# Optimization experiments

Hardware: AMD Instinct MI355X
Metric: run time of the kernel (lower is better)

The kernel has to match this reference:

```python
import jax, jax.numpy as jnp
import numpy as np

N_NODES = 50000
N_EDGES = 800000


def _sage(x, src, dst, Wl, bl, Wr):
    # mean-aggregate neighbor features (messages flow src -> dst), then linear
    msg = x[src]                                              # [E, d_in]
    s = jax.ops.segment_sum(msg, dst, num_segments=N_NODES)   # [N, d_in]
    cnt = jax.ops.segment_sum(jnp.ones((src.shape[0],), x.dtype), dst,
                              num_segments=N_NODES)           # [N]
    agg = s / jnp.maximum(cnt, 1.0)[:, None]
    return agg @ Wl.T + bl + x @ Wr.T


def setup_inputs() -> dict:
    key = jax.random.key(0)
    ks = jax.random.split(key, 10)
    d_in, h = 128, 64
    def w(k, o, i):
        return jax.random.normal(k, (o, i), jnp.float32) * (1.0 / np.sqrt(i))
    return {
        "x": jax.random.normal(ks[0], (N_NODES, d_in), jnp.float32),
        "edge_index": jax.random.randint(ks[1], (2, N_EDGES), 0, N_NODES, jnp.int64),
        "Wl1": w(ks[2], h, d_in), "bl1": jnp.zeros((h,), jnp.float32), "Wr1": w(ks[3], h, d_in),
        "Wl2": w(ks[4], 2 * h, h), "bl2": jnp.zeros((2 * h,), jnp.float32), "Wr2": w(ks[5], 2 * h, h),
        "Wl3": w(ks[6], 2 * h, 2 * h), "bl3": jnp.zeros((2 * h,), jnp.float32), "Wr3": w(ks[7], 2 * h, 2 * h),
        "Wl4": w(ks[8], h, 2 * h), "bl4": jnp.zeros((h,), jnp.float32), "Wr4": w(ks[9], h, 2 * h),
    }


def reference(x, edge_index, Wl1, bl1, Wr1, Wl2, bl2, Wr2, Wl3, bl3, Wr3, Wl4, bl4, Wr4):
    src, dst = edge_index[0], edge_index[1]
    h = jax.nn.relu(_sage(x, src, dst, Wl1, bl1, Wr1))
    h = jax.nn.relu(_sage(h, src, dst, Wl2, bl2, Wr2))
    h = jax.nn.relu(_sage(h, src, dst, Wl3, bl3, Wr3))
    h = _sage(h, src, dst, Wl4, bl4, Wr4)
    return h
```

## Files before the change

kernel.cpp:

```cpp
#include <hip/hip_runtime.h>

#define NN 50000
#define NE 800000
#define GB 391
#define NBUK 196
#define PB 128
#define CH 6250
#define HLEN (NBUK * PB)
#define SAB (HLEN / 256)

typedef __attribute__((ext_vector_type(8))) short short8v;
typedef __attribute__((ext_vector_type(4))) float float4v;

__device__ __forceinline__ int uni(int v) { return __builtin_amdgcn_readfirstlane(v); }
__device__ __forceinline__ unsigned short f2bf(float f) {
    unsigned u = __float_as_uint(f);
    return (unsigned short)((u + 0x7FFFu + ((u >> 16) & 1u)) >> 16);
}
__device__ __forceinline__ float bf2f(unsigned short h) {
    return __uint_as_float(((unsigned)h) << 16);
}

__global__ __launch_bounds__(256) void hist_kernel(const int* __restrict__ dst,
                                                   int* __restrict__ H) {
    __shared__ int h[NBUK];
    const int t = threadIdx.x;
    const int b = blockIdx.x;
    if (t < NBUK) h[t] = 0;
    __syncthreads();
    const int e0 = b * CH;
    for (int i = t; i < CH; i += 256) {
        int e = e0 + i;
        if (e < NE) atomicAdd(&h[dst[e] >> 8], 1);
    }
    __syncthreads();
    if (t < NBUK) H[t * PB + b] = h[t];
}

__global__ __launch_bounds__(256) void scanA_kernel(const int* __restrict__ a,
                                                    int* __restrict__ part) {
    __shared__ int red[256];
    const int t = threadIdx.x;
    red[t] = a[blockIdx.x * 256 + t];
    __syncthreads();
#pragma unroll
    for (int d = 128; d > 0; d >>= 1) {
        if (t < d) red[t] += red[t + d];
        __syncthreads();
    }
    if (t == 0) part[blockIdx.x] = red[0];
}

__global__ __launch_bounds__(128) void scanB_kernel(int* __restrict__ part) {
    __shared__ int ps[128];
    const int t = threadIdx.x;
    ps[t] = (t < SAB) ? part[t] : 0;
    __syncthreads();
#pragma unroll
    for (int d = 1; d < 128; d <<= 1) {
        int v = (t >= d) ? ps[t - d] : 0;
        __syncthreads();
        ps[t] += v;
        __syncthreads();
    }
    if (t < SAB) part[t] = (t == 0) ? 0 : ps[t - 1];
}

__global__ __launch_bounds__(256) void scanC_kernel(int* __restrict__ a,
                                                    const int* __restrict__ part) {
    __shared__ int ps[256];
    const int t = threadIdx.x;
    const int i = blockIdx.x * 256 + t;
    const int c = a[i];
    ps[t] = c;
    __syncthreads();
#pragma unroll
    for (int d = 1; d < 256; d <<= 1) {
        int v = (t >= d) ? ps[t - d] : 0;
        __syncthreads();
        ps[t] += v;
        __syncthreads();
    }
    a[i] = part[blockIdx.x] + ps[t] - c;
}

__global__ __launch_bounds__(256) void partition_kernel(const int* __restrict__ src,
                                                        const int* __restrict__ dst,
                                                        const int* __restrict__ Hs,
                                                        unsigned* __restrict__ tmp) {
    __shared__ int cur[NBUK];
    const int t = threadIdx.x;
    const int b = blockIdx.x;
    if (t < NBUK) cur[t] = Hs[t * PB + b];
    __syncthreads();
    const int e0 = b * CH;
    for (int i = t; i < CH; i += 256) {
        int e = e0 + i;
        if (e < NE) {
            const int d = dst[e];
            const int k = d >> 8;
            const int pos = atomicAdd(&cur[k], 1);
            tmp[pos] = (unsigned)src[e] | ((unsigned)(d & 255) << 16);
        }
    }
}

__global__ __launch_bounds__(256) void finalize_kernel(const unsigned* __restrict__ tmp,
                                                       const int* __restrict__ Hs,
                                                       int* __restrict__ off,
                                                       int* __restrict__ cnt,
                                                       float* __restrict__ inv,
                                                       int* __restrict__ srcs) {
    __shared__ int hist[256];
    __shared__ int ps[256];
    __shared__ int cur[256];
    const int t = threadIdx.x;
    const int k = blockIdx.x;
    const int s0 = Hs[k * PB];
    const int end = (k == NBUK - 1) ? NE : Hs[(k + 1) * PB];
    const int m = end - s0;
    hist[t] = 0;
    __syncthreads();
    for (int i = t; i < m; i += 256) {
        atomicAdd(&hist[(tmp[s0 + i] >> 16) & 255], 1);
    }
    __syncthreads();
    const int c = hist[t];
    ps[t] = c;
    __syncthreads();
#pragma unroll
    for (int d = 1; d < 256; d <<= 1) {
        int v = (t >= d) ? ps[t - d] : 0;
        __syncthreads();
        ps[t] += v;
        __syncthreads();
    }
    const int ex = ps[t] - c;
    const int node = k * 256 + t;
    if (node < NN) {
        off[node] = s0 + ex;
        cnt[node] = c;
        inv[node] = 1.0f / (float)max(c, 1);
    }
    cur[t] = s0 + ex;
    __syncthreads();
    for (int i = t; i < m; i += 256) {
        const unsigned u = tmp[s0 + i];
        const int p = atomicAdd(&cur[(u >> 16) & 255], 1);
        srcs[p] = (int)(u & 0xFFFFu);
    }
}

template<int D, int MODE, int DUALB>
__global__ __launch_bounds__(256) void gather_kernel(
    const unsigned short* __restrict__ yb, int ys, const int* __restrict__ srcs,
    const int* __restrict__ off, const int* __restrict__ cnt,
    const float* __restrict__ inv, const float* __restrict__ pre, int ps,
    float* __restrict__ out, int os, unsigned short* __restrict__ outb) {
    const int w = (blockIdx.x * blockDim.x + threadIdx.x) >> 6;
    const int lane = threadIdx.x & 63;
    if (w >= NN) return;
    const int o = uni(off[w]);
    const int n = uni(cnt[w]);
    const int h = lane >> 5;
    const int l = lane & 31;

    float a0 = 0.0f, a1 = 0.0f, a2 = 0.0f, a3 = 0.0f;
    int i = 0;
    for (; i + 8 <= n; i += 8) {
        int e0 = srcs[o + i + h];
        int e1 = srcs[o + i + 2 + h];
        int e2 = srcs[o + i + 4 + h];
        int e3 = srcs[o + i + 6 + h];
        if constexpr (D == 64) {
            const ushort2 v0 = *reinterpret_cast<const ushort2*>(&yb[(size_t)e0 * ys + 2 * l]);
            const ushort2 v1 = *reinterpret_cast<const ushort2*>(&yb[(size_t)e1 * ys + 2 * l]);
            const ushort2 v2 = *reinterpret_cast<const ushort2*>(&yb[(size_t)e2 * ys + 2 * l]);
            const ushort2 v3 = *reinterpret_cast<const ushort2*>(&yb[(size_t)e3 * ys + 2 * l]);
            a0 += bf2f(v0.x) + bf2f(v1.x) + bf2f(v2.x) + bf2f(v3.x);
            a1 += bf2f(v0.y) + bf2f(v1.y) + bf2f(v2.y) + bf2f(v3.y);
        } else {
            const ushort4 v0 = *reinterpret_cast<const ushort4*>(&yb[(size_t)e0 * ys + 4 * l]);
            const ushort4 v1 = *reinterpret_cast<const ushort4*>(&yb[(size_t)e1 * ys + 4 * l]);
            const ushort4 v2 = *reinterpret_cast<const ushort4*>(&yb[(size_t)e2 * ys + 4 * l]);
            const ushort4 v3 = *reinterpret_cast<const ushort4*>(&yb[(size_t)e3 * ys + 4 * l]);
            a0 += bf2f(v0.x) + bf2f(v1.x) + bf2f(v2.x) + bf2f(v3.x);
            a1 += bf2f(v0.y) + bf2f(v1.y) + bf2f(v2.y) + bf2f(v3.y);
            a2 += bf2f(v0.z) + bf2f(v1.z) + bf2f(v2.z) + bf2f(v3.z);
            a3 += bf2f(v0.w) + bf2f(v1.w) + bf2f(v2.w) + bf2f(v3.w);
        }
    }
    for (; i + 2 <= n; i += 2) {
        int e = srcs[o + i + h];
        if constexpr (D == 64) {
            const ushort2 v = *reinterpret_cast<const ushort2*>(&yb[(size_t)e * ys + 2 * l]);
            a0 += bf2f(v.x);
            a1 += bf2f(v.y);
        } else {
            const ushort4 v = *reinterpret_cast<const ushort4*>(&yb[(size_t)e * ys + 4 * l]);
            a0 += bf2f(v.x); a1 += bf2f(v.y); a2 += bf2f(v.z); a3 += bf2f(v.w);
        }
    }
    if (i < n && h == 0) {
        int e = srcs[o + i];
        if constexpr (D == 64) {
            const ushort2 v = *reinterpret_cast<const ushort2*>(&yb[(size_t)e * ys + 2 * l]);
            a0 += bf2f(v.x);
            a1 += bf2f(v.y);
        } else {
            const ushort4 v = *reinterpret_cast<const ushort4*>(&yb[(size_t)e * ys + 4 * l]);
            a0 += bf2f(v.x); a1 += bf2f(v.y); a2 += bf2f(v.z); a3 += bf2f(v.w);
        }
    }
    a0 += __shfl_xor(a0, 32, 64);
    a1 += __shfl_xor(a1, 32, 64);
    if constexpr (D == 128) {
        a2 += __shfl_xor(a2, 32, 64);
        a3 += __shfl_xor(a3, 32, 64);
    }
    if (h != 0) return;

    const float iv = inv[w];
    if constexpr (D == 64) {
        float r0 = a0 * iv, r1 = a1 * iv;
        if constexpr (MODE != 0) {
            const float2 pv = *reinterpret_cast<const float2*>(&pre[(size_t)w * ps + 2 * l]);
            r0 += pv.x; r1 += pv.y;
        }
        if constexpr (MODE == 1) { r0 = fmaxf(r0, 0.0f); r1 = fmaxf(r1, 0.0f); }
        float2 sv = {r0, r1};
        *reinterpret_cast<float2*>(&out[(size_t)w * os + 2 * l]) = sv;
        if constexpr (DUALB) {
            ushort2 bv = {f2bf(r0), f2bf(r1)};
            *reinterpret_cast<ushort2*>(&outb[(size_t)w * 64 + 2 * l]) = bv;
        }
    } else {
        float r0 = a0 * iv, r1 = a1 * iv, r2 = a2 * iv, r3 = a3 * iv;
        if constexpr (MODE != 0) {
            const float4 pv = *reinterpret_cast<const float4*>(&pre[(size_t)w * ps + 4 * l]);
            r0 += pv.x; r1 += pv.y; r2 += pv.z; r3 += pv.w;
        }
        if constexpr (MODE == 1) {
            r0 = fmaxf(r0, 0.0f); r1 = fmaxf(r1, 0.0f);
            r2 = fmaxf(r2, 0.0f); r3 = fmaxf(r3, 0.0f);
        }
        float4 sv = {r0, r1, r2, r3};
        *reinterpret_cast<float4*>(&out[(size_t)w * os + 4 * l]) = sv;
    }
}

struct WSrc { const float* p[8]; };

__global__ __launch_bounds__(256) void wplanes_kernel(WSrc S,
                                                      unsigned short* __restrict__ ph,
                                                      unsigned short* __restrict__ pl) {
    const int e = blockIdx.x * 256 + threadIdx.x;
    const int seg = blockIdx.y;
    const int row = e >> 7, k = e & 127;
    float x;
    switch (seg) {
        case 0:  x = (row < 64) ? S.p[0][row * 128 + k] : S.p[1][(row - 64) * 128 + k]; break;
        case 1:  x = (k < 64)   ? S.p[2][row * 64 + k]  : S.p[3][row * 64 + (k - 64)];  break;
        case 2:  x = S.p[4][e]; break;
        case 3:  x = S.p[5][e]; break;
        default: x = (row < 64) ? S.p[6][row * 128 + k] : S.p[7][(row - 64) * 128 + k]; break;
    }
    const unsigned u = __float_as_uint(x);
    const float lo = x - __uint_as_float(u & 0xFFFF0000u);
    const int o = seg * 16384 + e;
    ph[o] = (unsigned short)(u >> 16);
    pl[o] = (unsigned short)(__float_as_uint(lo) >> 16);
}

__global__ __launch_bounds__(256) void gemm_mfma(
    const float* __restrict__ in,
    const unsigned short* __restrict__ Bh, const unsigned short* __restrict__ Bl,
    float* __restrict__ out0, const float* __restrict__ bias0, int os0, int obf0,
    float* __restrict__ out1, const float* __restrict__ bias1, int os1, int obf1,
    int relu) {
    const int t = threadIdx.x;
    const int lane = t & 63;
    const int wid = t >> 6;
    const int wn = wid & 1;
    const int wc = wid >> 1;
    const int l15 = lane & 15;
    const int lk = lane >> 4;
    const int nb = (int)blockIdx.x * 128 + wn * 64;

    float* const outp = wc ? out1 : out0;
    const float* const biasp = wc ? bias1 : bias0;
    const int os = wc ? os1 : os0;
    const int obf = wc ? obf1 : obf0;
    const unsigned short* const Bhp = Bh + (size_t)(wc * 64) * 128;
    const unsigned short* const Blp = Bl + (size_t)(wc * 64) * 128;
    const ptrdiff_t dlo = Blp - Bhp;

    float4v acc[4][4];
#pragma unroll
    for (int mi = 0; mi < 4; ++mi)
#pragma unroll
        for (int ci = 0; ci < 4; ++ci) acc[mi][ci] = (float4v)0.0f;

    const float* arow[4];
#pragma unroll
    for (int mi = 0; mi < 4; ++mi) {
        int r = nb + mi * 16 + l15;
        if (r > NN - 1) r = NN - 1;
        arow[mi] = in + (size_t)r * 128;
    }
    const unsigned short* brow[4];
#pragma unroll
    for (int ci = 0; ci < 4; ++ci) brow[ci] = Bhp + (size_t)(ci * 16 + l15) * 128;

    for (int ks = 0; ks < 4; ++ks) {
        const int ko = ks * 32 + lk * 8;
        short8v Ah[4], Al[4];
#pragma unroll
        for (int mi = 0; mi < 4; ++mi) {
            const float4v v0 = *reinterpret_cast<const float4v*>(arow[mi] + ko);
            const float4v v1 = *reinterpret_cast<const float4v*>(arow[mi] + ko + 4);
            float xv[8] = {v0.x, v0.y, v0.z, v0.w, v1.x, v1.y, v1.z, v1.w};
            union { unsigned u[4]; short8v s; } H, L;
#pragma unroll
            for (int q = 0; q < 4; ++q) {
                const unsigned u0 = __float_as_uint(xv[2 * q]);
                const unsigned u1 = __float_as_uint(xv[2 * q + 1]);
                const float l0 = xv[2 * q]     - __uint_as_float(u0 & 0xFFFF0000u);
                const float l1 = xv[2 * q + 1] - __uint_as_float(u1 & 0xFFFF0000u);
                H.u[q] = (u1 & 0xFFFF0000u) | (u0 >> 16);
                L.u[q] = (__float_as_uint(l1) & 0xFFFF0000u) | (__float_as_uint(l0) >> 16);
            }
            Ah[mi] = H.s;
            Al[mi] = L.s;
        }
        short8v Bhf[4], Blf[4];
#pragma unroll
        for (int ci = 0; ci < 4; ++ci) {
            Bhf[ci] = *reinterpret_cast<const short8v*>(brow[ci] + ko);
            Blf[ci] = *reinterpret_cast<const short8v*>(brow[ci] + dlo + ko);
        }
#pragma unroll
        for (int mi = 0; mi < 4; ++mi)
#pragma unroll
            for (int ci = 0; ci < 4; ++ci) {
                acc[mi][ci] = __builtin_amdgcn_mfma_f32_16x16x32_bf16(Ah[mi], Bhf[ci], acc[mi][ci], 0, 0, 0);
                acc[mi][ci] = __builtin_amdgcn_mfma_f32_16x16x32_bf16(Ah[mi], Blf[ci], acc[mi][ci], 0, 0, 0);
                acc[mi][ci] = __builtin_amdgcn_mfma_f32_16x16x32_bf16(Al[mi], Bhf[ci], acc[mi][ci], 0, 0, 0);
            }
    }

#pragma unroll
    for (int ci = 0; ci < 4; ++ci) {
        const int c = ci * 16 + l15;
        const float b = biasp ? biasp[c] : 0.0f;
#pragma unroll
        for (int mi = 0; mi < 4; ++mi) {
#pragma unroll
            for (int j = 0; j < 4; ++j) {
                const int r = nb + mi * 16 + lk * 4 + j;
                if (r < NN) {
                    float v = acc[mi][ci][j] + b;
                    if (relu) v = fmaxf(v, 0.0f);
                    if (obf) ((unsigned short*)outp)[(size_t)r * os + c] = f2bf(v);
                    else outp[(size_t)r * os + c] = v;
                }
            }
        }
    }
}

extern "C" void kernel_launch(void* const* d_in, const int* in_sizes, int n_in,
                              void* d_out, int out_size, void* d_ws, size_t ws_size,
                              hipStream_t stream) {
    const float* x   = (const float*)d_in[0];
    const int*   eix = (const int*)d_in[1];
    const float* Wl1 = (const float*)d_in[2];
    const float* bl1 = (const float*)d_in[3];
    const float* Wr1 = (const float*)d_in[4];
    const float* Wl2 = (const float*)d_in[5];
    const float* bl2 = (const float*)d_in[6];
    const float* Wr2 = (const float*)d_in[7];
    const float* Wl3 = (const float*)d_in[8];
    const float* bl3 = (const float*)d_in[9];
    const float* Wr3 = (const float*)d_in[10];
    const float* Wl4 = (const float*)d_in[11];
    const float* bl4 = (const float*)d_in[12];
    const float* Wr4 = (const float*)d_in[13];
    float* out = (float*)d_out;

    const int* src = eix;
    const int* dst = eix + NE;

    char* ws = (char*)d_ws;
    int*   cnt  = (int*)ws;
    int*   off  = cnt + NN;
    float* inv  = (float*)(off + NN);
    int*   Hs   = (int*)(inv + NN);
    int*   part = Hs + HLEN;
    int*   srcs = part + 256;
    unsigned short* ph = (unsigned short*)(srcs + NE);
    unsigned short* pl = ph + 81920;
    unsigned short* XB1 = pl + 81920;
    unsigned short* H1B = XB1 + (size_t)NN * 64;
    unsigned short* G3B = XB1;
    float* HCAT = (float*)(XB1 + (size_t)NN * 128);
    float* H2   = HCAT + (size_t)NN * 128;
    float* HPRE = H2 + (size_t)NN * 128;
    unsigned*       tmp = (unsigned*)HPRE;
    unsigned short* G4B = (unsigned short*)HCAT;

    hist_kernel<<<PB, 256, 0, stream>>>(dst, Hs);
    scanA_kernel<<<SAB, 256, 0, stream>>>(Hs, part);
    scanB_kernel<<<1, 128, 0, stream>>>(part);
    scanC_kernel<<<SAB, 256, 0, stream>>>(Hs, part);
    partition_kernel<<<PB, 256, 0, stream>>>(src, dst, Hs, tmp);
    finalize_kernel<<<NBUK, 256, 0, stream>>>(tmp, Hs, off, cnt, inv, srcs);

    {
        WSrc s;
        s.p[0] = Wl1; s.p[1] = Wr1; s.p[2] = Wl2; s.p[3] = Wr2;
        s.p[4] = Wl3; s.p[5] = Wr3; s.p[6] = Wl4; s.p[7] = Wr4;
        wplanes_kernel<<<dim3(64, 5), 256, 0, stream>>>(s, ph, pl);
    }

    gemm_mfma<<<GB, 256, 0, stream>>>(x, ph, pl,
                                      (float*)XB1, nullptr, 64, 1,
                                      HCAT + 64, bl1, 128, 0, 0);
    gather_kernel<64, 1, 1><<<12500, 256, 0, stream>>>(
        XB1, 64, srcs, off, cnt, inv, HCAT + 64, 128, HCAT + 64, 128, H1B);

    gather_kernel<64, 0, 0><<<12500, 256, 0, stream>>>(
        H1B, 64, srcs, off, cnt, inv, nullptr, 0, HCAT, 128, nullptr);
    gemm_mfma<<<GB, 256, 0, stream>>>(HCAT, ph + 16384, pl + 16384,
                                      H2, bl2, 128, 0,
                                      H2 + 64, bl2 + 64, 128, 0, 1);

    gemm_mfma<<<GB, 256, 0, stream>>>(H2, ph + 2 * 16384, pl + 2 * 16384,
                                      (float*)G3B, nullptr, 128, 1,
                                      (float*)(G3B + 64), nullptr, 128, 1, 0);
    gemm_mfma<<<GB, 256, 0, stream>>>(H2, ph + 3 * 16384, pl + 3 * 16384,
                                      HPRE, bl3, 128, 0,
                                      HPRE + 64, bl3 + 64, 128, 0, 0);
    gather_kernel<128, 1, 0><<<12500, 256, 0, stream>>>(
        G3B, 128, srcs, off, cnt, inv, HPRE, 128, HPRE, 128, nullptr);

    gemm_mfma<<<GB, 256, 0, stream>>>(HPRE, ph + 4 * 16384, pl + 4 * 16384,
                                      (float*)G4B, nullptr, 64, 1,
                                      out, bl4, 64, 0, 0);
    gather_kernel<64, 2, 0><<<12500, 256, 0, stream>>>(
        G4B, 64, srcs, off, cnt, inv, out, 64, out, 64, nullptr);
}
```

Before: 323.9 us.

## Shard gather kernel by feature columns and store neighbor indices as 16-bit

The gather is split so each wave handles a 32-column shard of a node's features: 2 shards for 64-wide layers and 4 for 128-wide. The grid is enlarged and block ids are interleaved so that blocks working on the same column shard run close together, with the aim of keeping each shard's slice of the feature table resident in cache. Neighbor source indices are also narrowed from int to unsigned short to halve index traffic. The cost is that every wave now re-reads offsets, counts and indices once per shard and does scalar 2-byte loads instead of vector loads. The 16-bit indices also cannot represent node ids at or above 65536; N_NODES is 50000, so they fit here.

```diff
diff --git a/kernel.cpp b/kernel.cpp
--- a/kernel.cpp
+++ b/kernel.cpp
@@ -8,6 +8,8 @@
 #define CH 6250
 #define HLEN (NBUK * PB)
 #define SAB (HLEN / 256)
+#define GS64 25000
+#define GS128 50000
 
 typedef __attribute__((ext_vector_type(8))) short short8v;
 typedef __attribute__((ext_vector_type(4))) float float4v;
@@ -110,7 +112,7 @@
                                                        int* __restrict__ off,
                                                        int* __restrict__ cnt,
                                                        float* __restrict__ inv,
-                                                       int* __restrict__ srcs) {
+                                                       unsigned short* __restrict__ srcs) {
     __shared__ int hist[256];
     __shared__ int ps[256];
     __shared__ int cur[256];
@@ -147,106 +149,63 @@
     for (int i = t; i < m; i += 256) {
         const unsigned u = tmp[s0 + i];
         const int p = atomicAdd(&cur[(u >> 16) & 255], 1);
-        srcs[p] = (int)(u & 0xFFFFu);
+        srcs[p] = (unsigned short)(u & 0xFFFFu);
     }
 }
 
 template<int D, int MODE, int DUALB>
 __global__ __launch_bounds__(256) void gather_kernel(
-    const unsigned short* __restrict__ yb, int ys, const int* __restrict__ srcs,
+    const unsigned short* __restrict__ yb, int ys, const unsigned short* __restrict__ srcs,
     const int* __restrict__ off, const int* __restrict__ cnt,
     const float* __restrict__ inv, const float* __restrict__ pre, int ps,
     float* __restrict__ out, int os, unsigned short* __restrict__ outb) {
-    const int w = (blockIdx.x * blockDim.x + threadIdx.x) >> 6;
+    const int bid = (int)blockIdx.x;
+    const int wid = threadIdx.x >> 6;
     const int lane = threadIdx.x & 63;
+    int shard, j;
+    if constexpr (D == 64) {
+        shard = (bid & 7) >> 2;
+        j = (bid >> 3) * 4 + (bid & 3);
+    } else {
+        shard = (bid & 7) >> 1;
+        j = (bid >> 3) * 2 + (bid & 1);
+    }
+    const int w = j * 4 + wid;
     if (w >= NN) return;
     const int o = uni(off[w]);
     const int n = uni(cnt[w]);
     const int h = lane >> 5;
     const int l = lane & 31;
-
-    float a0 = 0.0f, a1 = 0.0f, a2 = 0.0f, a3 = 0.0f;
+    const int col = shard * 32 + l;
+
+    float a0 = 0.0f;
     int i = 0;
     for (; i + 8 <= n; i += 8) {
         int e0 = srcs[o + i + h];
         int e1 = srcs[o + i + 2 + h];
         int e2 = srcs[o + i + 4 + h];
         int e3 = srcs[o + i + 6 + h];
-        if constexpr (D == 64) {
-            const ushort2 v0 = *reinterpret_cast<const ushort2*>(&yb[(size_t)e0 * ys + 2 * l]);
-            const ushort2 v1 = *reinterpret_cast<const ushort2*>(&yb[(size_t)e1 * ys + 2 * l]);
-            const ushort2 v2 = *reinterpret_cast<const ushort2*>(&yb[(size_t)e2 * ys + 2 * l]);
-            const ushort2 v3 = *reinterpret_cast<const ushort2*>(&yb[(size_t)e3 * ys + 2 * l]);
-            a0 += bf2f(v0.x) + bf2f(v1.x) + bf2f(v2.x) + bf2f(v3.x);
-            a1 += bf2f(v0.y) + bf2f(v1.y) + bf2f(v2.y) + bf2f(v3.y);
-        } else {
-            const ushort4 v0 = *reinterpret_cast<const ushort4*>(&yb[(size_t)e0 * ys + 4 * l]);
-            const ushort4 v1 = *reinterpret_cast<const ushort4*>(&yb[(size_t)e1 * ys + 4 * l]);
-            const ushort4 v2 = *reinterpret_cast<const ushort4*>(&yb[(size_t)e2 * ys + 4 * l]);
-            const ushort4 v3 = *reinterpret_cast<const ushort4*>(&yb[(size_t)e3 * ys + 4 * l]);
-            a0 += bf2f(v0.x) + bf2f(v1.x) + bf2f(v2.x) + bf2f(v3.x);
-            a1 += bf2f(v0.y) + bf2f(v1.y) + bf2f(v2.y) + bf2f(v3.y);
-            a2 += bf2f(v0.z) + bf2f(v1.z) + bf2f(v2.z) + bf2f(v3.z);
-            a3 += bf2f(v0.w) + bf2f(v1.w) + bf2f(v2.w) + bf2f(v3.w);
-        }
+        a0 += bf2f(yb[(size_t)e0 * ys + col]);
+        a0 += bf2f(yb[(size_t)e1 * ys + col]);
+        a0 += bf2f(yb[(size_t)e2 * ys + col]);
+        a0 += bf2f(yb[(size_t)e3 * ys + col]);
     }
     for (; i + 2 <= n; i += 2) {
         int e = srcs[o + i + h];
-        if constexpr (D == 64) {
-            const ushort2 v = *reinterpret_cast<const ushort2*>(&yb[(size_t)e * ys + 2 * l]);
-            a0 += bf2f(v.x);
-            a1 += bf2f(v.y);
-        } else {
-            const ushort4 v = *reinterpret_cast<const ushort4*>(&yb[(size_t)e * ys + 4 * l]);
-            a0 += bf2f(v.x); a1 += bf2f(v.y); a2 += bf2f(v.z); a3 += bf2f(v.w);
-        }
+        a0 += bf2f(yb[(size_t)e * ys + col]);
     }
     if (i < n && h == 0) {
         int e = srcs[o + i];
-        if constexpr (D == 64) {
-            const ushort2 v = *reinterpret_cast<const ushort2*>(&yb[(size_t)e * ys + 2 * l]);
-            a0 += bf2f(v.x);
-            a1 += bf2f(v.y);
-        } else {
-            const ushort4 v = *reinterpret_cast<const ushort4*>(&yb[(size_t)e * ys + 4 * l]);
-            a0 += bf2f(v.x); a1 += bf2f(v.y); a2 += bf2f(v.z); a3 += bf2f(v.w);
-        }
+        a0 += bf2f(yb[(size_t)e * ys + col]);
     }
     a0 += __shfl_xor(a0, 32, 64);
-    a1 += __shfl_xor(a1, 32, 64);
-    if constexpr (D == 128) {
-        a2 += __shfl_xor(a2, 32, 64);
-        a3 += __shfl_xor(a3, 32, 64);
-    }
     if (h != 0) return;
 
-    const float iv = inv[w];
-    if constexpr (D == 64) {
-        float r0 = a0 * iv, r1 = a1 * iv;
-        if constexpr (MODE != 0) {
-            const float2 pv = *reinterpret_cast<const float2*>(&pre[(size_t)w * ps + 2 * l]);
-            r0 += pv.x; r1 += pv.y;
-        }
-        if constexpr (MODE == 1) { r0 = fmaxf(r0, 0.0f); r1 = fmaxf(r1, 0.0f); }
-        float2 sv = {r0, r1};
-        *reinterpret_cast<float2*>(&out[(size_t)w * os + 2 * l]) = sv;
-        if constexpr (DUALB) {
-            ushort2 bv = {f2bf(r0), f2bf(r1)};
-            *reinterpret_cast<ushort2*>(&outb[(size_t)w * 64 + 2 * l]) = bv;
-        }
-    } else {
-        float r0 = a0 * iv, r1 = a1 * iv, r2 = a2 * iv, r3 = a3 * iv;
-        if constexpr (MODE != 0) {
-            const float4 pv = *reinterpret_cast<const float4*>(&pre[(size_t)w * ps + 4 * l]);
-            r0 += pv.x; r1 += pv.y; r2 += pv.z; r3 += pv.w;
-        }
-        if constexpr (MODE == 1) {
-            r0 = fmaxf(r0, 0.0f); r1 = fmaxf(r1, 0.0f);
-            r2 = fmaxf(r2, 0.0f); r3 = fmaxf(r3, 0.0f);
-        }
-        float4 sv = {r0, r1, r2, r3};
-        *reinterpret_cast<float4*>(&out[(size_t)w * os + 4 * l]) = sv;
-    }
+    float r0 = a0 * inv[w];
+    if constexpr (MODE != 0) r0 += pre[(size_t)w * ps + col];
+    if constexpr (MODE == 1) r0 = fmaxf(r0, 0.0f);
+    out[(size_t)w * os + col] = r0;
+    if constexpr (DUALB) outb[(size_t)w * 64 + col] = f2bf(r0);
 }
 
 struct WSrc { const float* p[8]; };
@@ -397,8 +356,8 @@
     float* inv  = (float*)(off + NN);
     int*   Hs   = (int*)(inv + NN);
     int*   part = Hs + HLEN;
-    int*   srcs = part + 256;
-    unsigned short* ph = (unsigned short*)(srcs + NE);
+    unsigned short* srcs = (unsigned short*)(part + 256);
+    unsigned short* ph = srcs + NE;
     unsigned short* pl = ph + 81920;
     unsigned short* XB1 = pl + 81920;
     unsigned short* H1B = XB1 + (size_t)NN * 64;
@@ -426,10 +385,10 @@
     gemm_mfma<<<GB, 256, 0, stream>>>(x, ph, pl,
                                       (float*)XB1, nullptr, 64, 1,
                                       HCAT + 64, bl1, 128, 0, 0);
-    gather_kernel<64, 1, 1><<<12500, 256, 0, stream>>>(
+    gather_kernel<64, 1, 1><<<GS64, 256, 0, stream>>>(
         XB1, 64, srcs, off, cnt, inv, HCAT + 64, 128, HCAT + 64, 128, H1B);
 
-    gather_kernel<64, 0, 0><<<12500, 256, 0, stream>>>(
+    gather_kernel<64, 0, 0><<<GS64, 256, 0, stream>>>(
         H1B, 64, srcs, off, cnt, inv, nullptr, 0, HCAT, 128, nullptr);
     gemm_mfma<<<GB, 256, 0, stream>>>(HCAT, ph + 16384, pl + 16384,
                                       H2, bl2, 128, 0,
@@ -441,12 +400,12 @@
     gemm_mfma<<<GB, 256, 0, stream>>>(H2, ph + 3 * 16384, pl + 3 * 16384,
                                       HPRE, bl3, 128, 0,
                                       HPRE + 64, bl3 + 64, 128, 0, 0);
-    gather_kernel<128, 1, 0><<<12500, 256, 0, stream>>>(
+    gather_kernel<128, 1, 0><<<GS128, 256, 0, stream>>>(
         G3B, 128, srcs, off, cnt, inv, HPRE, 128, HPRE, 128, nullptr);
 
     gemm_mfma<<<GB, 256, 0, stream>>>(HPRE, ph + 4 * 16384, pl + 4 * 16384,
                                       (float*)G4B, nullptr, 64, 1,
                                       out, bl4, 64, 0, 0);
-    gather_kernel<64, 2, 0><<<12500, 256, 0, stream>>>(
+    gather_kernel<64, 2, 0><<<GS64, 256, 0, stream>>>(
         G4B, 64, srcs, off, cnt, inv, out, 64, out, 64, nullptr);
 }
```

Result: slower. 436.5 us (+34.8%).
